# Optimization experiments

Measured on AMD Instinct MI355X. Metric: run time of the kernel, lower is better.

Reference implementation:

```python
import jax, jax.numpy as jnp
import numpy as np

MARGIN = 0.3
N = 8192
D = 256
NUM_CLASSES = 64


def setup_inputs() -> dict:
    key = jax.random.key(0)
    k1, k2 = jax.random.split(key)
    embeddings = jax.random.normal(k1, (N, D), dtype=jnp.float32)
    labels = jax.random.randint(k2, (N,), 0, NUM_CLASSES, dtype=jnp.int64)
    return {"embeddings": embeddings, "labels": labels}


def _pairwise_euclidean(x):
    # torch.cdist(x, x, p=2): sqrt of squared distances, safe at 0
    sq = jnp.sum(x * x, axis=-1)                       # [N]
    d2 = sq[:, None] + sq[None, :] - 2.0 * (x @ x.T)   # [N, N]
    d2 = jnp.maximum(d2, 0.0)
    pos = d2 > 0
    return jnp.where(pos, jnp.sqrt(jnp.where(pos, d2, 1.0)), 0.0)


def reference(embeddings, labels):
    d = _pairwise_euclidean(embeddings)                # [N, N]
    same = labels[:, None] == labels[None, :]          # [N, N] pos_mask (incl. self)
    neg = ~same                                        # neg_mask
    pos_nz = same & (d > 0.0)                          # pos_dist[pos_dist > 0]

    hardest_pos = jnp.max(jnp.where(pos_nz, d, -jnp.inf), axis=1)  # [N]
    hardest_neg = jnp.min(jnp.where(neg, d, jnp.inf), axis=1)      # [N]

    # valid anchors: >1 positives (incl. self), >=1 negative, and a nonzero pos dist
    valid = (jnp.sum(same, axis=1) > 1) & jnp.any(neg, axis=1) & jnp.any(pos_nz, axis=1)

    per_anchor = jnp.where(valid,
                           jax.nn.relu(hardest_pos - hardest_neg + MARGIN),
                           0.0)
    count = jnp.sum(valid.astype(jnp.float32))
    return jnp.where(count > 0,
                     jnp.sum(per_anchor) / jnp.maximum(count, 1.0),
                     0.0)
```

## Files before the change

### kernel.cpp

```cpp
#include <hip/hip_runtime.h>


#define N_PTS 8192
#define DIM   256
#define MARGIN 0.3f

typedef __attribute__((ext_vector_type(8))) short bf16x8;
typedef __attribute__((ext_vector_type(4))) float f32x4;

__device__ __forceinline__ unsigned short f2bf(float f) {
    unsigned u = __float_as_uint(f);
    u += 0x7FFFu + ((u >> 16) & 1u);
    return (unsigned short)(u >> 16);
}

__global__ void prep_kernel(const float* __restrict__ X,
                            unsigned short* __restrict__ Xb,
                            float* __restrict__ sq) {
    int t = blockIdx.x * 256 + threadIdx.x;
    {
        int row = t >> 6, lane = t & 63;
        float4 v = reinterpret_cast<const float4*>(X)[t];
        float p = v.x * v.x + v.y * v.y + v.z * v.z + v.w * v.w;
        #pragma unroll
        for (int m = 1; m < 64; m <<= 1) p += __shfl_xor(p, m, 64);
        if (lane == 0) sq[row] = p;
    }
    {
        int i    = t & 1023;
        int Rg   = t >> 10;
        int half = i & 1;
        int lsub = (i >> 1) & 15;
        int lgrp = (i >> 5) & 3;
        int kk   = (i >> 7) & 7;
        int row  = Rg * 16 + lsub;
        int sidx = row * 64 + kk * 8 + lgrp * 2 + half;
        float4 v = reinterpret_cast<const float4*>(X)[sidx];
        ushort4 b4;
        b4.x = f2bf(v.x); b4.y = f2bf(v.y); b4.z = f2bf(v.z); b4.w = f2bf(v.w);
        reinterpret_cast<ushort4*>(Xb)[t] = b4;
    }
}

__launch_bounds__(512, 2)
__global__ void mine_kernel(const unsigned short* __restrict__ Xb,
                            const float* __restrict__ sq,
                            const int* __restrict__ labels,
                            float* __restrict__ vp,
                            float* __restrict__ vn) {
    int bid = blockIdx.x;
    int panel = bid >> 2;
    int q     = bid & 3;
    int tid = threadIdx.x;
    int w = tid >> 6, l = tid & 63;
    int wr = w >> 2, wc = w & 3;
    int lsub = l & 15, lgrp = l >> 4;

    const float INF = __int_as_float(0x7f800000);

    const unsigned short* abase = Xb + (size_t)(panel * 8 + wr * 4) * 4096 + l * 8;
    bf16x8 a[4][8];
    #pragma unroll
    for (int m = 0; m < 4; ++m)
        #pragma unroll
        for (int kk = 0; kk < 8; ++kk)
            a[m][kk] = *reinterpret_cast<const bf16x8*>(abase + m * 4096 + kk * 512);

    int rowbase = panel * 128 + wr * 64;
    int lrj[4][4];
    #pragma unroll
    for (int m = 0; m < 4; ++m)
        #pragma unroll
        for (int j = 0; j < 4; ++j)
            lrj[m][j] = labels[rowbase + m * 16 + lgrp * 4 + j];

    float vpr[4][4], vnr[4][4];
    #pragma unroll
    for (int m = 0; m < 4; ++m)
        #pragma unroll
        for (int j = 0; j < 4; ++j) { vpr[m][j] = -INF; vnr[m][j] = INF; }

    int colwave = q * 2048 + wc * 512;
    const unsigned short* bbase = Xb + (size_t)(colwave >> 4) * 4096 + l * 8;

    for (int cs = 0; cs < 16; ++cs) {
        int colbase = colwave + cs * 32;
        int lc0 = labels[colbase + lsub];
        int lc1 = labels[colbase + 16 + lsub];
        float sc0 = sq[colbase + lsub];
        float sc1 = sq[colbase + 16 + lsub];

        f32x4 acc[4][2];
        #pragma unroll
        for (int m = 0; m < 4; ++m) {
            acc[m][0] = (f32x4){0.f, 0.f, 0.f, 0.f};
            acc[m][1] = (f32x4){0.f, 0.f, 0.f, 0.f};
        }

        const unsigned short* bb = bbase + (size_t)cs * 8192;
        #pragma unroll
        for (int kp = 0; kp < 4; ++kp) {
            bf16x8 b00 = *reinterpret_cast<const bf16x8*>(bb + kp * 1024);
            bf16x8 b01 = *reinterpret_cast<const bf16x8*>(bb + 4096 + kp * 1024);
            bf16x8 b10 = *reinterpret_cast<const bf16x8*>(bb + kp * 1024 + 512);
            bf16x8 b11 = *reinterpret_cast<const bf16x8*>(bb + 4096 + kp * 1024 + 512);
            #pragma unroll
            for (int m = 0; m < 4; ++m) {
                acc[m][0] = __builtin_amdgcn_mfma_f32_16x16x32_bf16(
                    a[m][2 * kp], b00, acc[m][0], 0, 0, 0);
                acc[m][1] = __builtin_amdgcn_mfma_f32_16x16x32_bf16(
                    a[m][2 * kp], b01, acc[m][1], 0, 0, 0);
            }
            #pragma unroll
            for (int m = 0; m < 4; ++m) {
                acc[m][0] = __builtin_amdgcn_mfma_f32_16x16x32_bf16(
                    a[m][2 * kp + 1], b10, acc[m][0], 0, 0, 0);
                acc[m][1] = __builtin_amdgcn_mfma_f32_16x16x32_bf16(
                    a[m][2 * kp + 1], b11, acc[m][1], 0, 0, 0);
            }
        }

        #pragma unroll
        for (int m = 0; m < 4; ++m)
            #pragma unroll
            for (int j = 0; j < 4; ++j) {
                int lr = lrj[m][j];
                float v0 = fmaf(-2.f, acc[m][0][j], sc0);
                float v1 = fmaf(-2.f, acc[m][1][j], sc1);
                bool s0 = (lr == lc0), s1 = (lr == lc1);
                vpr[m][j] = fmaxf(vpr[m][j], s0 ? v0 : -INF);
                vpr[m][j] = fmaxf(vpr[m][j], s1 ? v1 : -INF);
                vnr[m][j] = fminf(vnr[m][j], s0 ? INF : v0);
                vnr[m][j] = fminf(vnr[m][j], s1 ? INF : v1);
            }
    }

    int slot = q * 4 + wc;
    #pragma unroll
    for (int m = 0; m < 4; ++m)
        #pragma unroll
        for (int j = 0; j < 4; ++j) {
            float p = vpr[m][j], n = vnr[m][j];
            #pragma unroll
            for (int s = 1; s < 16; s <<= 1) {
                p = fmaxf(p, __shfl_xor(p, s, 64));
                n = fminf(n, __shfl_xor(n, s, 64));
            }
            if (lsub == 0) {
                int row = rowbase + m * 16 + lgrp * 4 + j;
                vp[slot * N_PTS + row] = p;
                vn[slot * N_PTS + row] = n;
            }
        }
}

__global__ void finalizeA_kernel(const float* __restrict__ vp,
                                 const float* __restrict__ vn,
                                 const float* __restrict__ sq,
                                 const int* __restrict__ labels,
                                 float* __restrict__ bsum,
                                 float* __restrict__ bcnt) {
    __shared__ int hist[64];
    __shared__ float ss[4], cc[4];
    int tid = threadIdx.x;
    if (tid < 64) hist[tid] = 0;
    __syncthreads();
    for (int i = tid; i < N_PTS; i += 256) atomicAdd(&hist[labels[i]], 1);
    __syncthreads();

    const float INF = __int_as_float(0x7f800000);
    int r = blockIdx.x * 256 + tid;
    float mp = -INF, mn = INF;
    #pragma unroll
    for (int s = 0; s < 16; ++s) {
        mp = fmaxf(mp, vp[s * N_PTS + r]);
        mn = fminf(mn, vn[s * N_PTS + r]);
    }
    float sr = sq[r];
    float hp2 = sr + mp;
    float hn2 = fmaxf(sr + mn, 0.f);
    int h = hist[labels[r]];
    bool valid = (h > 1) && (h < N_PTS) && (hp2 > 0.f);
    float contrib = valid ? fmaxf(sqrtf(hp2) - sqrtf(hn2) + MARGIN, 0.f) : 0.f;
    float cnt = valid ? 1.f : 0.f;

    #pragma unroll
    for (int m = 1; m < 64; m <<= 1) {
        contrib += __shfl_xor(contrib, m, 64);
        cnt     += __shfl_xor(cnt, m, 64);
    }
    int wv = tid >> 6, lv = tid & 63;
    if (lv == 0) { ss[wv] = contrib; cc[wv] = cnt; }
    __syncthreads();
    if (tid == 0) {
        bsum[blockIdx.x] = ss[0] + ss[1] + ss[2] + ss[3];
        bcnt[blockIdx.x] = cc[0] + cc[1] + cc[2] + cc[3];
    }
}

__global__ void finalizeB_kernel(const float* __restrict__ bsum,
                                 const float* __restrict__ bcnt,
                                 float* __restrict__ out) {
    int l = threadIdx.x;
    float s = (l < 32) ? bsum[l] : 0.f;
    float c = (l < 32) ? bcnt[l] : 0.f;
    #pragma unroll
    for (int m = 1; m < 64; m <<= 1) {
        s += __shfl_xor(s, m, 64);
        c += __shfl_xor(c, m, 64);
    }
    if (l == 0) out[0] = (c > 0.f) ? (s / c) : 0.f;
}

extern "C" void kernel_launch(void* const* d_in, const int* in_sizes, int n_in,
                              void* d_out, int out_size, void* d_ws, size_t ws_size,
                              hipStream_t stream) {
    const float* X      = (const float*)d_in[0];
    const int*   labels = (const int*)d_in[1];
    float*       out    = (float*)d_out;

    char* ws = (char*)d_ws;
    unsigned short* Xb = (unsigned short*)ws;
    float* sq   = (float*)(ws + 4194304);
    float* vp   = (float*)(ws + 4194304 + 32768);
    float* vn   = (float*)(ws + 4194304 + 32768 + 524288);
    float* bsum = (float*)(ws + 4194304 + 32768 + 1048576);
    float* bcnt = (float*)(ws + 4194304 + 32768 + 1048576 + 128);

    prep_kernel<<<2048, 256, 0, stream>>>(X, Xb, sq);
    mine_kernel<<<256, 512, 0, stream>>>(Xb, sq, labels, vp, vn);
    finalizeA_kernel<<<32, 256, 0, stream>>>(vp, vn, sq, labels, bsum, bcnt);
    finalizeB_kernel<<<1, 64, 0, stream>>>(bsum, bcnt, out);
}
```

Baseline: 112.9 us.

## Retile mining kernel for more blocks and restage bf16 prep through LDS

The prep kernel now converts 32 rows per block into a padded LDS tile and writes the MFMA-swizzled bf16 layout from shared memory, so global reads are fully coalesced. The mining kernel halves each wave's row tile (2 m-blocks instead of 4), splits columns into 8 slices instead of 4, doubles the grid to 512 blocks, and raises the occupancy target to 4 blocks per CU. Block IDs are swizzled so neighbouring blocks share column ranges. Smaller tiles cut register pressure and improve CU coverage, at the cost of less A-register reuse per B load and more B traffic per MFMA.

```diff
diff --git a/kernel.cpp b/kernel.cpp
--- a/kernel.cpp
+++ b/kernel.cpp
@@ -14,73 +14,83 @@
     return (unsigned short)(u >> 16);
 }
 
-__global__ void prep_kernel(const float* __restrict__ X,
-                            unsigned short* __restrict__ Xb,
-                            float* __restrict__ sq) {
-    int t = blockIdx.x * 256 + threadIdx.x;
-    {
-        int row = t >> 6, lane = t & 63;
-        float4 v = reinterpret_cast<const float4*>(X)[t];
+__global__ __launch_bounds__(256)
+void prep_kernel(const float* __restrict__ X,
+                 unsigned short* __restrict__ Xb,
+                 float* __restrict__ sq) {
+    __shared__ unsigned short lds[32][264];
+    int t = threadIdx.x;
+    int w = t >> 6, l = t & 63;
+    int blk = blockIdx.x;
+    int row0 = blk * 32;
+    #pragma unroll
+    for (int i = 0; i < 8; ++i) {
+        int r = i * 4 + w;
+        float4 v = reinterpret_cast<const float4*>(X)[(size_t)(row0 + r) * 64 + l];
+        ushort4 b;
+        b.x = f2bf(v.x); b.y = f2bf(v.y); b.z = f2bf(v.z); b.w = f2bf(v.w);
+        *reinterpret_cast<ushort4*>(&lds[r][l * 4]) = b;
         float p = v.x * v.x + v.y * v.y + v.z * v.z + v.w * v.w;
         #pragma unroll
         for (int m = 1; m < 64; m <<= 1) p += __shfl_xor(p, m, 64);
-        if (lane == 0) sq[row] = p;
-    }
-    {
-        int i    = t & 1023;
-        int Rg   = t >> 10;
-        int half = i & 1;
-        int lsub = (i >> 1) & 15;
-        int lgrp = (i >> 5) & 3;
-        int kk   = (i >> 7) & 7;
-        int row  = Rg * 16 + lsub;
-        int sidx = row * 64 + kk * 8 + lgrp * 2 + half;
-        float4 v = reinterpret_cast<const float4*>(X)[sidx];
-        ushort4 b4;
-        b4.x = f2bf(v.x); b4.y = f2bf(v.y); b4.z = f2bf(v.z); b4.w = f2bf(v.w);
-        reinterpret_cast<ushort4*>(Xb)[t] = b4;
-    }
-}
-
-__launch_bounds__(512, 2)
+        if (l == 0) sq[row0 + r] = p;
+    }
+    __syncthreads();
+    #pragma unroll
+    for (int j = 0; j < 8; ++j) {
+        int i = j * 256 + t;
+        int ii = i & 1023;
+        int Rg = i >> 10;
+        int kk = ii >> 7;
+        int ll = (ii >> 1) & 63;
+        int half = ii & 1;
+        int r = Rg * 16 + (ll & 15);
+        int k = kk * 32 + (ll >> 4) * 8 + half * 4;
+        ushort4 b = *reinterpret_cast<const ushort4*>(&lds[r][k]);
+        reinterpret_cast<ushort4*>(Xb)[(size_t)blk * 2048 + i] = b;
+    }
+}
+
+__launch_bounds__(512, 4)
 __global__ void mine_kernel(const unsigned short* __restrict__ Xb,
                             const float* __restrict__ sq,
                             const int* __restrict__ labels,
                             float* __restrict__ vp,
                             float* __restrict__ vn) {
     int bid = blockIdx.x;
-    int panel = bid >> 2;
-    int q     = bid & 3;
+    int swz = (bid & 7) * 64 + (bid >> 3);
+    int panel = swz >> 3;
+    int e     = swz & 7;
     int tid = threadIdx.x;
     int w = tid >> 6, l = tid & 63;
-    int wr = w >> 2, wc = w & 3;
+    int wr = w >> 1, wc = w & 1;
     int lsub = l & 15, lgrp = l >> 4;
 
     const float INF = __int_as_float(0x7f800000);
 
-    const unsigned short* abase = Xb + (size_t)(panel * 8 + wr * 4) * 4096 + l * 8;
-    bf16x8 a[4][8];
-    #pragma unroll
-    for (int m = 0; m < 4; ++m)
+    const unsigned short* abase = Xb + (size_t)(panel * 8 + wr * 2) * 4096 + l * 8;
+    bf16x8 a[2][8];
+    #pragma unroll
+    for (int m = 0; m < 2; ++m)
         #pragma unroll
         for (int kk = 0; kk < 8; ++kk)
             a[m][kk] = *reinterpret_cast<const bf16x8*>(abase + m * 4096 + kk * 512);
 
-    int rowbase = panel * 128 + wr * 64;
-    int lrj[4][4];
-    #pragma unroll
-    for (int m = 0; m < 4; ++m)
+    int rowbase = panel * 128 + wr * 32;
+    int lrj[2][4];
+    #pragma unroll
+    for (int m = 0; m < 2; ++m)
         #pragma unroll
         for (int j = 0; j < 4; ++j)
             lrj[m][j] = labels[rowbase + m * 16 + lgrp * 4 + j];
 
-    float vpr[4][4], vnr[4][4];
-    #pragma unroll
-    for (int m = 0; m < 4; ++m)
+    float vpr[2][4], vnr[2][4];
+    #pragma unroll
+    for (int m = 0; m < 2; ++m)
         #pragma unroll
         for (int j = 0; j < 4; ++j) { vpr[m][j] = -INF; vnr[m][j] = INF; }
 
-    int colwave = q * 2048 + wc * 512;
+    int colwave = e * 1024 + wc * 512;
     const unsigned short* bbase = Xb + (size_t)(colwave >> 4) * 4096 + l * 8;
 
     for (int cs = 0; cs < 16; ++cs) {
@@ -90,9 +100,9 @@
         float sc0 = sq[colbase + lsub];
         float sc1 = sq[colbase + 16 + lsub];
 
-        f32x4 acc[4][2];
-        #pragma unroll
-        for (int m = 0; m < 4; ++m) {
+        f32x4 acc[2][2];
+        #pragma unroll
+        for (int m = 0; m < 2; ++m) {
             acc[m][0] = (f32x4){0.f, 0.f, 0.f, 0.f};
             acc[m][1] = (f32x4){0.f, 0.f, 0.f, 0.f};
         }
@@ -105,14 +115,14 @@
             bf16x8 b10 = *reinterpret_cast<const bf16x8*>(bb + kp * 1024 + 512);
             bf16x8 b11 = *reinterpret_cast<const bf16x8*>(bb + 4096 + kp * 1024 + 512);
             #pragma unroll
-            for (int m = 0; m < 4; ++m) {
+            for (int m = 0; m < 2; ++m) {
                 acc[m][0] = __builtin_amdgcn_mfma_f32_16x16x32_bf16(
                     a[m][2 * kp], b00, acc[m][0], 0, 0, 0);
                 acc[m][1] = __builtin_amdgcn_mfma_f32_16x16x32_bf16(
                     a[m][2 * kp], b01, acc[m][1], 0, 0, 0);
             }
             #pragma unroll
-            for (int m = 0; m < 4; ++m) {
+            for (int m = 0; m < 2; ++m) {
                 acc[m][0] = __builtin_amdgcn_mfma_f32_16x16x32_bf16(
                     a[m][2 * kp + 1], b10, acc[m][0], 0, 0, 0);
                 acc[m][1] = __builtin_amdgcn_mfma_f32_16x16x32_bf16(
@@ -121,7 +131,7 @@
         }
 
         #pragma unroll
-        for (int m = 0; m < 4; ++m)
+        for (int m = 0; m < 2; ++m)
             #pragma unroll
             for (int j = 0; j < 4; ++j) {
                 int lr = lrj[m][j];
@@ -135,9 +145,9 @@
             }
     }
 
-    int slot = q * 4 + wc;
-    #pragma unroll
-    for (int m = 0; m < 4; ++m)
+    int slot = e * 2 + wc;
+    #pragma unroll
+    for (int m = 0; m < 2; ++m)
         #pragma unroll
         for (int j = 0; j < 4; ++j) {
             float p = vpr[m][j], n = vnr[m][j];
@@ -227,8 +237,8 @@
     float* bsum = (float*)(ws + 4194304 + 32768 + 1048576);
     float* bcnt = (float*)(ws + 4194304 + 32768 + 1048576 + 128);
 
-    prep_kernel<<<2048, 256, 0, stream>>>(X, Xb, sq);
-    mine_kernel<<<256, 512, 0, stream>>>(Xb, sq, labels, vp, vn);
+    prep_kernel<<<256, 256, 0, stream>>>(X, Xb, sq);
+    mine_kernel<<<512, 512, 0, stream>>>(Xb, sq, labels, vp, vn);
     finalizeA_kernel<<<32, 256, 0, stream>>>(vp, vn, sq, labels, bsum, bcnt);
     finalizeB_kernel<<<1, 64, 0, stream>>>(bsum, bcnt, out);
 }
```

New measurement: 138.2 us. 1.22x slower.
